# Performance work log

Hardware: AMD Instinct MI355X
Metric: run time of the kernel (lower is better)

Reference implementation:

```python
import jax, jax.numpy as jnp
import numpy as np

N_NODES = 100000
IN_DIM = 128
HIDDEN = 64
N_EDGES = 1600000


def setup_inputs() -> dict:
    key = jax.random.key(0)
    k_z, k_e, k_w1, k_b1, k_w2, k_b2 = jax.random.split(key, 6)
    z = jax.random.normal(k_z, (N_NODES, IN_DIM), dtype=jnp.float32)
    edge_index = jax.random.randint(k_e, (2, N_EDGES), 0, N_NODES, dtype=jnp.int64)
    # PyTorch Linear stores weight [out, in]; keep [in, out] layout for x @ W
    bound1 = 1.0 / np.sqrt(2 * IN_DIM)
    W1 = jax.random.uniform(k_w1, (2 * IN_DIM, HIDDEN), jnp.float32, -bound1, bound1)
    b1 = jax.random.uniform(k_b1, (HIDDEN,), jnp.float32, -bound1, bound1)
    bound2 = 1.0 / np.sqrt(HIDDEN)
    W2 = jax.random.uniform(k_w2, (HIDDEN, 1), jnp.float32, -bound2, bound2)
    b2 = jax.random.uniform(k_b2, (1,), jnp.float32, -bound2, bound2)
    return {"z": z, "edge_index": edge_index, "W1": W1, "b1": b1, "W2": W2, "b2": b2}


def reference(z, edge_index, W1, b1, W2, b2):
    src = edge_index[0]
    dst = edge_index[1]
    # gather node features and concat: [E, 2*D]
    edge_feat = jnp.concatenate([z[src], z[dst]], axis=-1)
    h = jax.nn.relu(edge_feat @ W1 + b1)  # [E, H]
    logits = h @ W2 + b2                  # [E, 1]
    return jax.nn.sigmoid(logits).squeeze(-1)  # [E]
```

## Files before the change

kernel.cpp:

```cpp
#include <hip/hip_runtime.h>
#include <hip/hip_bf16.h>

#define N_NODES 100000
#define IN_DIM  128
#define HIDDEN  64
#define N_EDGES 1600000

typedef unsigned short u16;
typedef unsigned int   u32;

typedef __attribute__((ext_vector_type(8))) short bf16x8;
typedef __attribute__((ext_vector_type(4))) float f32x4;

__device__ __forceinline__ u16 f2bf(float f) {
    u32 u = __float_as_uint(f);
    u32 r = 0x7FFFu + ((u >> 16) & 1u);
    u += r;
    return (u16)(u >> 16);
}

__global__ __launch_bounds__(256) void prep_kernel(const float* __restrict__ W1,
                                                   u16* __restrict__ WcatT) {
    int idx = blockIdx.x * 256 + threadIdx.x;
    int jj = idx >> 7;
    int k  = idx & 127;
    float v = (jj < 64) ? W1[k * 64 + jj] : W1[(128 + k) * 64 + (jj - 64)];
    WcatT[idx] = f2bf(v);
}

#define MT  64
#define LDK 136

__global__ __launch_bounds__(256) void gemm_kernel(const float* __restrict__ z,
                                                   const u16* __restrict__ WcatT,
                                                   const float* __restrict__ b1,
                                                   u16* __restrict__ UV) {
    __shared__ u16 As[MT * LDK];
    __shared__ u16 Bs[128 * LDK];

    int tid = threadIdx.x;
    int m0  = blockIdx.x * MT;

    for (int c = tid; c < 128 * 16; c += 256) {
        int row = c >> 4, cc = c & 15;
        uint4 v = *(const uint4*)(WcatT + row * 128 + cc * 8);
        *(uint4*)(Bs + row * LDK + cc * 8) = v;
    }
    for (int c = tid; c < MT * 32; c += 256) {
        int row = c >> 5, cc = c & 31;
        int gm = m0 + row;
        if (gm >= N_NODES) gm = N_NODES - 1;
        float4 f = *(const float4*)(z + (size_t)gm * 128 + cc * 4);
        u32 lo = (u32)f2bf(f.x) | ((u32)f2bf(f.y) << 16);
        u32 hi = (u32)f2bf(f.z) | ((u32)f2bf(f.w) << 16);
        uint2 val; val.x = lo; val.y = hi;
        *(uint2*)(As + row * LDK + cc * 4) = val;
    }
    __syncthreads();

    int wave = tid >> 6;
    int lane = tid & 63;
    int quad = lane >> 4;
    int l16  = lane & 15;

    f32x4 acc[8];
    const f32x4 z4 = {0.f, 0.f, 0.f, 0.f};
#pragma unroll
    for (int i = 0; i < 8; i++) acc[i] = z4;

    int arow = wave * 16 + l16;
#pragma unroll
    for (int kb = 0; kb < 4; kb++) {
        int k0 = kb * 32 + quad * 8;
        bf16x8 a = *(const bf16x8*)(As + arow * LDK + k0);
#pragma unroll
        for (int nt = 0; nt < 8; nt++) {
            bf16x8 b = *(const bf16x8*)(Bs + (nt * 16 + l16) * LDK + k0);
            acc[nt] = __builtin_amdgcn_mfma_f32_16x16x32_bf16(a, b, acc[nt], 0, 0, 0);
        }
    }

#pragma unroll
    for (int nt = 0; nt < 8; nt++) {
        int col = nt * 16 + l16;
        float bias = (col < HIDDEN) ? b1[col] : 0.f;
#pragma unroll
        for (int r = 0; r < 4; r++) {
            int row = m0 + wave * 16 + quad * 4 + r;
            if (row < N_NODES) {
                UV[(size_t)row * 128 + col] = f2bf(acc[nt][r] + bias);
            }
        }
    }
}

#define EDGE_ITERS 8
#define BATCH 4

__global__ __launch_bounds__(256) void edge_kernel(const int* __restrict__ ei,
                                                   const u16* __restrict__ UV,
                                                   const float* __restrict__ W2,
                                                   const float* __restrict__ b2,
                                                   float* __restrict__ out) {
    int gwave = (blockIdx.x * 256 + threadIdx.x) >> 6;
    int lane  = threadIdx.x & 63;
    int sub   = lane >> 3;
    int c     = lane & 7;

    float4 w2a = *(const float4*)(W2 + c * 8);
    float4 w2b = *(const float4*)(W2 + c * 8 + 4);
    float w2r[8] = {w2a.x, w2a.y, w2a.z, w2a.w, w2b.x, w2b.y, w2b.z, w2b.w};
    float b2v = b2[0];

    int ebase = gwave * (8 * EDGE_ITERS) + sub;

#pragma unroll
    for (int it4 = 0; it4 < EDGE_ITERS; it4 += BATCH) {
        int sB[BATCH], dB[BATCH];
#pragma unroll
        for (int j = 0; j < BATCH; j++) {
            int e = ebase + (it4 + j) * 8;
            sB[j] = ei[e];
            dB[j] = ei[N_EDGES + e];
        }
        uint4 aB[BATCH], bB[BATCH];
#pragma unroll
        for (int j = 0; j < BATCH; j++) {
            aB[j] = *(const uint4*)(UV + (size_t)sB[j] * 128 + c * 8);
            bB[j] = *(const uint4*)(UV + (size_t)dB[j] * 128 + 64 + c * 8);
        }
#pragma unroll
        for (int j = 0; j < BATCH; j++) {
            u32 aw[4] = {aB[j].x, aB[j].y, aB[j].z, aB[j].w};
            u32 bw[4] = {bB[j].x, bB[j].y, bB[j].z, bB[j].w};
            float acc = 0.f;
#pragma unroll
            for (int i = 0; i < 4; i++) {
                float u0 = __uint_as_float(aw[i] << 16);
                float u1 = __uint_as_float(aw[i] & 0xFFFF0000u);
                float v0 = __uint_as_float(bw[i] << 16);
                float v1 = __uint_as_float(bw[i] & 0xFFFF0000u);
                float h0 = fmaxf(u0 + v0, 0.f);
                float h1 = fmaxf(u1 + v1, 0.f);
                acc = fmaf(h0, w2r[i * 2], acc);
                acc = fmaf(h1, w2r[i * 2 + 1], acc);
            }
            acc += __shfl_xor(acc, 1);
            acc += __shfl_xor(acc, 2);
            acc += __shfl_xor(acc, 4);
            if (c == 0) {
                int e = ebase + (it4 + j) * 8;
                float x = acc + b2v;
                out[e] = 1.f / (1.f + __expf(-x));
            }
        }
    }
}

extern "C" void kernel_launch(void* const* d_in, const int* in_sizes, int n_in,
                              void* d_out, int out_size, void* d_ws, size_t ws_size,
                              hipStream_t stream) {
    const float* z  = (const float*)d_in[0];
    const int*   ei = (const int*)d_in[1];
    const float* W1 = (const float*)d_in[2];
    const float* b1 = (const float*)d_in[3];
    const float* W2 = (const float*)d_in[4];
    const float* b2 = (const float*)d_in[5];
    float* out = (float*)d_out;

    u16* WcatT = (u16*)d_ws;
    u16* UV    = (u16*)((char*)d_ws + 65536);

    prep_kernel<<<64, 256, 0, stream>>>(W1, WcatT);
    gemm_kernel<<<(N_NODES + MT - 1) / MT, 256, 0, stream>>>(z, WcatT, b1, UV);
    edge_kernel<<<6250, 256, 0, stream>>>(ei, UV, W2, b2, out);
}
```

Measured before the change: 170.3 us.

## Make node GEMM persistent with A fragments loaded directly into registers

The node GEMM now launches a fixed grid of 625 blocks in which each wave loops over 16-row tiles. The weight tile is staged in LDS once per block instead of once per 64 rows. A fragments are read straight from global memory into registers and converted to bf16 there, which removes the A staging in LDS. In exchange the global loads for A are strided per lane and less coalesced, and the loop relies on N_NODES being divisible by 16.

```diff
diff --git a/kernel.cpp b/kernel.cpp
--- a/kernel.cpp
+++ b/kernel.cpp
@@ -28,33 +28,19 @@
     WcatT[idx] = f2bf(v);
 }
 
-#define MT  64
 #define LDK 136
+#define GEMM_BLOCKS 625
 
 __global__ __launch_bounds__(256) void gemm_kernel(const float* __restrict__ z,
                                                    const u16* __restrict__ WcatT,
                                                    const float* __restrict__ b1,
                                                    u16* __restrict__ UV) {
-    __shared__ u16 As[MT * LDK];
     __shared__ u16 Bs[128 * LDK];
 
     int tid = threadIdx.x;
-    int m0  = blockIdx.x * MT;
-
     for (int c = tid; c < 128 * 16; c += 256) {
         int row = c >> 4, cc = c & 15;
-        uint4 v = *(const uint4*)(WcatT + row * 128 + cc * 8);
-        *(uint4*)(Bs + row * LDK + cc * 8) = v;
-    }
-    for (int c = tid; c < MT * 32; c += 256) {
-        int row = c >> 5, cc = c & 31;
-        int gm = m0 + row;
-        if (gm >= N_NODES) gm = N_NODES - 1;
-        float4 f = *(const float4*)(z + (size_t)gm * 128 + cc * 4);
-        u32 lo = (u32)f2bf(f.x) | ((u32)f2bf(f.y) << 16);
-        u32 hi = (u32)f2bf(f.z) | ((u32)f2bf(f.w) << 16);
-        uint2 val; val.x = lo; val.y = hi;
-        *(uint2*)(As + row * LDK + cc * 4) = val;
+        *(uint4*)(Bs + row * LDK + cc * 8) = *(const uint4*)(WcatT + row * 128 + cc * 8);
     }
     __syncthreads();
 
@@ -63,32 +49,57 @@
     int quad = lane >> 4;
     int l16  = lane & 15;
 
-    f32x4 acc[8];
-    const f32x4 z4 = {0.f, 0.f, 0.f, 0.f};
+    int gwid   = blockIdx.x * 4 + wave;
+    int nwaves = GEMM_BLOCKS * 4;
+    const int NTILES = N_NODES / 16;
+
+    float bias[4];
 #pragma unroll
-    for (int i = 0; i < 8; i++) acc[i] = z4;
+    for (int nt = 0; nt < 4; nt++) bias[nt] = b1[nt * 16 + l16];
 
-    int arow = wave * 16 + l16;
+    for (int t = gwid; t < NTILES; t += nwaves) {
+        const float* zrow = z + (size_t)(t * 16 + l16) * 128;
+
+        float4 fa[8];
 #pragma unroll
-    for (int kb = 0; kb < 4; kb++) {
-        int k0 = kb * 32 + quad * 8;
-        bf16x8 a = *(const bf16x8*)(As + arow * LDK + k0);
+        for (int kb = 0; kb < 4; kb++) {
+            fa[kb * 2]     = *(const float4*)(zrow + kb * 32 + quad * 8);
+            fa[kb * 2 + 1] = *(const float4*)(zrow + kb * 32 + quad * 8 + 4);
+        }
+        bf16x8 afrag[4];
+#pragma unroll
+        for (int kb = 0; kb < 4; kb++) {
+            union { bf16x8 v; u32 w[4]; } pk;
+            float4 lo = fa[kb * 2], hi = fa[kb * 2 + 1];
+            pk.w[0] = (u32)f2bf(lo.x) | ((u32)f2bf(lo.y) << 16);
+            pk.w[1] = (u32)f2bf(lo.z) | ((u32)f2bf(lo.w) << 16);
+            pk.w[2] = (u32)f2bf(hi.x) | ((u32)f2bf(hi.y) << 16);
+            pk.w[3] = (u32)f2bf(hi.z) | ((u32)f2bf(hi.w) << 16);
+            afrag[kb] = pk.v;
+        }
+
+        f32x4 acc[8];
+        const f32x4 z4 = {0.f, 0.f, 0.f, 0.f};
+#pragma unroll
+        for (int i = 0; i < 8; i++) acc[i] = z4;
+
+#pragma unroll
+        for (int kb = 0; kb < 4; kb++) {
+            int k0 = kb * 32 + quad * 8;
+#pragma unroll
+            for (int nt = 0; nt < 8; nt++) {
+                bf16x8 b = *(const bf16x8*)(Bs + (nt * 16 + l16) * LDK + k0);
+                acc[nt] = __builtin_amdgcn_mfma_f32_16x16x32_bf16(afrag[kb], b, acc[nt], 0, 0, 0);
+            }
+        }
+
 #pragma unroll
         for (int nt = 0; nt < 8; nt++) {
-            bf16x8 b = *(const bf16x8*)(Bs + (nt * 16 + l16) * LDK + k0);
-            acc[nt] = __builtin_amdgcn_mfma_f32_16x16x32_bf16(a, b, acc[nt], 0, 0, 0);
-        }
-    }
-
+            float bb = (nt < 4) ? bias[nt] : 0.f;
 #pragma unroll
-    for (int nt = 0; nt < 8; nt++) {
-        int col = nt * 16 + l16;
-        float bias = (col < HIDDEN) ? b1[col] : 0.f;
-#pragma unroll
-        for (int r = 0; r < 4; r++) {
-            int row = m0 + wave * 16 + quad * 4 + r;
-            if (row < N_NODES) {
-                UV[(size_t)row * 128 + col] = f2bf(acc[nt][r] + bias);
+            for (int r = 0; r < 4; r++) {
+                int row = t * 16 + quad * 4 + r;
+                UV[(size_t)row * 128 + nt * 16 + l16] = f2bf(acc[nt][r] + bb);
             }
         }
     }
@@ -172,6 +183,6 @@
     u16* UV    = (u16*)((char*)d_ws + 65536);
 
     prep_kernel<<<64, 256, 0, stream>>>(W1, WcatT);
-    gemm_kernel<<<(N_NODES + MT - 1) / MT, 256, 0, stream>>>(z, WcatT, b1, UV);
+    gemm_kernel<<<GEMM_BLOCKS, 256, 0, stream>>>(z, WcatT, b1, UV);
     edge_kernel<<<6250, 256, 0, stream>>>(ei, UV, W2, b2, out);
 }
```

Result: faster. 164.2 us (-3.6%).
